# Kernel tuning notes

Hardware: AMD Instinct MI355X
Metric: run time of the kernel (lower is better)

The kernel has to match this reference:

```python
import jax, jax.numpy as jnp
import numpy as np

B, L_SRC, H = 16, 2048, 1024


def setup_inputs() -> dict:
    key = jax.random.key(0)
    ks = jax.random.split(key, 12)
    s = 1.0 / np.sqrt(H)
    return {
        "query": jax.random.normal(ks[0], (B, 1, H), jnp.float32),
        "states": jax.random.normal(ks[1], (B, L_SRC, H), jnp.float32),
        "states_features": jax.random.normal(ks[2], (B, L_SRC, H), jnp.float32),
        "coverage": jax.random.uniform(ks[3], (B, L_SRC, 1), jnp.float32),
        "source_mask": jax.random.randint(ks[4], (B, L_SRC), 0, 2, jnp.int32),
        "is_coverage": 1,
        "Wq": jax.random.normal(ks[5], (H, H), jnp.float32) * s,
        "bq": jax.random.normal(ks[6], (H,), jnp.float32) * s,
        "Wc": jax.random.normal(ks[7], (1, H), jnp.float32) * s,
        "v": jax.random.normal(ks[8], (H, 1), jnp.float32) * s,
        "Wout": jax.random.normal(ks[9], (H, 2 * H), jnp.float32) * s,
        "bout": jax.random.normal(ks[10], (H,), jnp.float32) * s,
    }


def reference(query, states, states_features, coverage, source_mask, is_coverage,
              Wq, bq, Wc, v, Wout, bout):
    # query: (B,1,H); states/states_features: (B,L,H); coverage: (B,L,1)
    query_features = query @ Wq.T + bq                       # (B,1,H), broadcasts over L
    total = query_features + states_features                 # (B,L,H)
    if is_coverage:
        total = total + coverage @ Wc                        # Linear(1,H), no bias
    alignments = jnp.tanh(total) @ v                         # (B,L,1)
    mask = source_mask.astype(bool)[:, :, None]              # (B,L,1)
    alignments = jnp.where(mask, alignments, -jnp.inf)
    align_vectors = jax.nn.softmax(alignments, axis=1)       # softmax over L_src
    c = jnp.einsum('bls,blh->bsh', align_vectors, states)    # (B,1,H)
    concat_c = jnp.concatenate([c, query], axis=2)           # (B,1,2H)
    attn_h = concat_c @ Wout.T + bout                         # (B,1,H)
    new_coverage = coverage + align_vectors
    return attn_h, new_coverage, align_vectors
```

## Files before the change

kernel.cpp:

```cpp
#include <hip/hip_runtime.h>
#include <cfloat>

#define HD 1024
#define LS 2048
#define NB 16
#define NCH 128
#define LPER (LS / NCH)

struct f4 { float x, y, z, w; };

__device__ inline f4 ld4(const float* p) { return *reinterpret_cast<const f4*>(p); }

__device__ inline float ftanh(float x) {
    x = fminf(10.f, fmaxf(-10.f, x));
    float t = __expf(2.f * x);
    return 1.f - 2.f * __builtin_amdgcn_rcpf(t + 1.f);
}

__device__ inline float dotTanh(const f4& s, const f4& q, const f4& wc, const f4& v, float covs) {
    return ftanh(s.x + q.x + covs * wc.x) * v.x
         + ftanh(s.y + q.y + covs * wc.y) * v.y
         + ftanh(s.z + q.z + covs * wc.z) * v.z
         + ftanh(s.w + q.w + covs * wc.w) * v.w;
}

__device__ inline float waveReduce(float v) {
    #pragma unroll
    for (int off = 32; off; off >>= 1) v += __shfl_xor(v, off, 64);
    return v;
}

__global__ void qf_kernel(const float* __restrict__ query, const float* __restrict__ Wq,
                          const float* __restrict__ bq, float* __restrict__ qf) {
    int h = blockIdx.x;
    int tid = threadIdx.x;
    int wv = tid >> 6, lane = tid & 63;
    int k0 = tid * 4;
    f4 w = ld4(Wq + (size_t)h * HD + k0);
    __shared__ float red[4][NB];
    float acc[NB];
    #pragma unroll
    for (int b = 0; b < NB; ++b) {
        f4 q = ld4(query + b * HD + k0);
        acc[b] = w.x * q.x + w.y * q.y + w.z * q.z + w.w * q.w;
    }
    #pragma unroll
    for (int b = 0; b < NB; ++b) {
        float r = waveReduce(acc[b]);
        if (lane == 0) red[wv][b] = r;
    }
    __syncthreads();
    if (tid < NB) {
        float s = red[0][tid] + red[1][tid] + red[2][tid] + red[3][tid];
        qf[tid * HD + h] = s + bq[h];
    }
}

__global__ __launch_bounds__(256) void fusedEC_kernel(
    const float* __restrict__ sf, const float* __restrict__ qf,
    const float* __restrict__ Wc, const float* __restrict__ vv,
    const float* __restrict__ coverage, const int* __restrict__ mask,
    const int* __restrict__ is_cov_p, const float* __restrict__ states,
    float* __restrict__ e_out, float* __restrict__ cpart)
{
    int chunk = blockIdx.x;
    int b = blockIdx.y;
    int tid = threadIdx.x;
    int wv = tid >> 6, lane = tid & 63;
    int l4 = lane * 4;
    int base_row = b * LS + chunk * LPER;
    int row0 = base_row + wv * 4;

    __shared__ float e_loc[LPER];

    int covflag = *is_cov_p;
    int4 mk = *reinterpret_cast<const int4*>(mask + row0);
    bool m0 = mk.x != 0, m1 = mk.y != 0, m2 = mk.z != 0, m3 = mk.w != 0;
    float cov0 = (covflag && m0) ? coverage[row0 + 0] : 0.f;
    float cov1 = (covflag && m1) ? coverage[row0 + 1] : 0.f;
    float cov2 = (covflag && m2) ? coverage[row0 + 2] : 0.f;
    float cov3 = (covflag && m3) ? coverage[row0 + 3] : 0.f;

    const float* qfr = qf + b * HD + l4;
    const float* ps = sf + (size_t)row0 * HD + l4;
    float a0 = 0.f, a1 = 0.f, a2 = 0.f, a3 = 0.f;

    #pragma unroll
    for (int it = 0; it < 4; ++it) {
        int o = it * 256;
        f4 q  = ld4(qfr + o);
        f4 wc = ld4(Wc + o + l4);
        f4 vf = ld4(vv + o + l4);
        f4 s0, s1, s2, s3;
        if (m0) s0 = ld4(ps + o);
        if (m1) s1 = ld4(ps + HD + o);
        if (m2) s2 = ld4(ps + 2 * HD + o);
        if (m3) s3 = ld4(ps + 3 * HD + o);
        if (m0) a0 += dotTanh(s0, q, wc, vf, cov0);
        if (m1) a1 += dotTanh(s1, q, wc, vf, cov1);
        if (m2) a2 += dotTanh(s2, q, wc, vf, cov2);
        if (m3) a3 += dotTanh(s3, q, wc, vf, cov3);
    }

    #pragma unroll
    for (int off = 32; off; off >>= 1) {
        a0 += __shfl_xor(a0, off, 64);
        a1 += __shfl_xor(a1, off, 64);
        a2 += __shfl_xor(a2, off, 64);
        a3 += __shfl_xor(a3, off, 64);
    }
    if (lane == 0) {
        f4 o;
        o.x = m0 ? a0 : -1e30f;
        o.y = m1 ? a1 : -1e30f;
        o.z = m2 ? a2 : -1e30f;
        o.w = m3 ? a3 : -1e30f;
        *reinterpret_cast<f4*>(e_out + row0) = o;
        e_loc[wv * 4 + 0] = o.x;
        e_loc[wv * 4 + 1] = o.y;
        e_loc[wv * 4 + 2] = o.z;
        e_loc[wv * 4 + 3] = o.w;
    }
    __syncthreads();

    __shared__ float wq[LPER];
    __shared__ int ridx[LPER];
    __shared__ int snnz;
    if (tid < 64) {
        float ev = (tid < LPER) ? e_loc[tid] : -1e30f;
        float w = __expf(ev);
        unsigned long long bm = __ballot(w != 0.f);
        if (w != 0.f) {
            int pos = __popcll(bm & ((1ull << tid) - 1));
            wq[pos] = w;
            ridx[pos] = tid;
        }
        if (tid == 0) snnz = __popcll(bm);
    }
    __syncthreads();
    int nnz = snnz;
    int h0 = tid * 4;
    const float* sbase = states + (size_t)base_row * HD + h0;
    float ax = 0.f, ay = 0.f, az = 0.f, aw = 0.f;
    for (int i = 0; i < nnz; i += 4) {
        int j1 = i + 1, j2 = i + 2, j3 = i + 3;
        float w0 = wq[i];
        int   r0 = ridx[i];
        float w1 = (j1 < nnz) ? wq[j1] : 0.f;
        int   r1 = (j1 < nnz) ? ridx[j1] : r0;
        float w2 = (j2 < nnz) ? wq[j2] : 0.f;
        int   r2 = (j2 < nnz) ? ridx[j2] : r0;
        float w3 = (j3 < nnz) ? wq[j3] : 0.f;
        int   r3 = (j3 < nnz) ? ridx[j3] : r0;
        f4 s0 = ld4(sbase + ((size_t)r0 << 10));
        f4 s1 = ld4(sbase + ((size_t)r1 << 10));
        f4 s2 = ld4(sbase + ((size_t)r2 << 10));
        f4 s3 = ld4(sbase + ((size_t)r3 << 10));
        ax = fmaf(w0, s0.x, ax); ay = fmaf(w0, s0.y, ay); az = fmaf(w0, s0.z, az); aw = fmaf(w0, s0.w, aw);
        ax = fmaf(w1, s1.x, ax); ay = fmaf(w1, s1.y, ay); az = fmaf(w1, s1.z, az); aw = fmaf(w1, s1.w, aw);
        ax = fmaf(w2, s2.x, ax); ay = fmaf(w2, s2.y, ay); az = fmaf(w2, s2.z, az); aw = fmaf(w2, s2.w, aw);
        ax = fmaf(w3, s3.x, ax); ay = fmaf(w3, s3.y, ay); az = fmaf(w3, s3.z, az); aw = fmaf(w3, s3.w, aw);
    }
    f4 o; o.x = ax; o.y = ay; o.z = az; o.w = aw;
    *reinterpret_cast<f4*>(cpart + ((size_t)(b * NCH + chunk)) * HD + h0) = o;
}

__global__ __launch_bounds__(1024) void mid_kernel(
    const float* __restrict__ e, const float* __restrict__ coverage,
    const float* __restrict__ cpart, float* __restrict__ scale,
    float* __restrict__ csum, float* __restrict__ out_align, float* __restrict__ out_newcov)
{
    __shared__ float redm[16], reds[16];
    __shared__ float red4[4][256];
    if (blockIdx.x < 16) {
        int b = blockIdx.x;
        int t = threadIdx.x;
        int wv = t >> 6, lane = t & 63;
        float v0 = e[b * LS + t];
        float v1 = e[b * LS + t + 1024];
        float mx = fmaxf(v0, v1);
        #pragma unroll
        for (int off = 32; off; off >>= 1) mx = fmaxf(mx, __shfl_xor(mx, off, 64));
        if (lane == 0) redm[wv] = mx;
        __syncthreads();
        mx = redm[0];
        #pragma unroll
        for (int i = 1; i < 16; ++i) mx = fmaxf(mx, redm[i]);
        float e0 = __expf(v0 - mx), e1 = __expf(v1 - mx);
        float s = e0 + e1;
        #pragma unroll
        for (int off = 32; off; off >>= 1) s += __shfl_xor(s, off, 64);
        if (lane == 0) reds[wv] = s;
        __syncthreads();
        s = 0.f;
        #pragma unroll
        for (int i = 0; i < 16; ++i) s += reds[i];
        float invZ = 1.f / s;
        if (t == 0) scale[b] = __expf(-mx) * invZ;
        int i0 = b * LS + t, i1 = i0 + 1024;
        float p0 = e0 * invZ, p1 = e1 * invZ;
        out_align[i0] = p0;
        out_align[i1] = p1;
        out_newcov[i0] = coverage[i0] + p0;
        out_newcov[i1] = coverage[i1] + p1;
    } else {
        int blk = blockIdx.x - 16;
        int tt = threadIdx.x & 255;
        int g = threadIdx.x >> 8;
        int elem = blk * 256 + tt;
        int b = elem >> 10, h = elem & 1023;
        const float* p = cpart + (((size_t)(b * NCH + g * 32)) << 10) + h;
        float s = 0.f;
        #pragma unroll
        for (int ch = 0; ch < 32; ++ch) s += p[(size_t)ch << 10];
        red4[g][tt] = s;
        __syncthreads();
        if (g == 0) csum[elem] = red4[0][tt] + red4[1][tt] + red4[2][tt] + red4[3][tt];
    }
}

__global__ void out_kernel(const float* __restrict__ csum, const float* __restrict__ query,
                           const float* __restrict__ Wout, const float* __restrict__ bout,
                           const float* __restrict__ scale, float* __restrict__ attn) {
    int h = blockIdx.x;
    int tid = threadIdx.x;
    int wv = tid >> 6, lane = tid & 63;
    int j0 = tid * 8;
    const float* wr = Wout + (size_t)h * (2 * HD);
    f4 w0 = ld4(wr + j0);
    f4 w1 = ld4(wr + j0 + 4);
    const float* src = (j0 < HD) ? (csum + j0) : (query + j0 - HD);
    __shared__ float red[4][NB];
    float acc[NB];
    #pragma unroll
    for (int b = 0; b < NB; ++b) {
        f4 x0 = ld4(src + b * HD);
        f4 x1 = ld4(src + b * HD + 4);
        acc[b] = w0.x * x0.x + w0.y * x0.y + w0.z * x0.z + w0.w * x0.w
               + w1.x * x1.x + w1.y * x1.y + w1.z * x1.z + w1.w * x1.w;
    }
    #pragma unroll
    for (int b = 0; b < NB; ++b) {
        float r = waveReduce(acc[b]);
        if (lane == 0) red[wv][b] = r;
    }
    __syncthreads();
    if (tid < NB) {
        float cpartial = red[0][tid] + red[1][tid];
        float qpartial = red[2][tid] + red[3][tid];
        attn[tid * HD + h] = cpartial * scale[tid] + qpartial + bout[h];
    }
}

extern "C" void kernel_launch(void* const* d_in, const int* in_sizes, int n_in,
                              void* d_out, int out_size, void* d_ws, size_t ws_size,
                              hipStream_t stream) {
    const float* query    = (const float*)d_in[0];
    const float* states   = (const float*)d_in[1];
    const float* sf       = (const float*)d_in[2];
    const float* coverage = (const float*)d_in[3];
    const int*   mask     = (const int*)d_in[4];
    const int*   is_cov   = (const int*)d_in[5];
    const float* Wq       = (const float*)d_in[6];
    const float* bq       = (const float*)d_in[7];
    const float* Wc       = (const float*)d_in[8];
    const float* v        = (const float*)d_in[9];
    const float* Wout     = (const float*)d_in[10];
    const float* bout     = (const float*)d_in[11];

    float* out      = (float*)d_out;
    float* attn     = out;
    float* newcov   = out + 16384;
    float* alignout = out + 49152;

    float* w  = (float*)d_ws;
    float* qf      = w;
    float* e       = w + 16384;
    float* cpart   = w + 49152;
    float* scale   = w + 49152 + 2097152;
    float* csum    = scale + 16;

    qf_kernel<<<dim3(HD), dim3(256), 0, stream>>>(query, Wq, bq, qf);
    fusedEC_kernel<<<dim3(NCH, NB), dim3(256), 0, stream>>>(
        sf, qf, Wc, v, coverage, mask, is_cov, states, e, cpart);
    mid_kernel<<<dim3(80), dim3(1024), 0, stream>>>(e, coverage, cpart, scale, csum, alignout, newcov);
    out_kernel<<<dim3(HD), dim3(256), 0, stream>>>(csum, query, Wout, bout, scale, attn);
}
```

Measured before the change: 56.80 us.

## Stage unmasked feature and state rows into LDS via async global_load_lds

The fused energy/context kernel now reads the mask first, compacts the unmasked row indices, and copies only those rows of states_features into a 64 KB shared buffer using direct global-to-LDS loads. It computes energies from LDS, then reuses the same buffer to stage the needed states rows before the weighted context sum. The aim is to issue the memory traffic asynchronously and in bulk, keeping it off the register path, and to skip masked rows early. The cost is 64 KB of LDS per block, which limits occupancy to about one or two blocks per CU, plus extra barriers that serialize load and compute phases.

```diff
diff --git a/kernel.cpp b/kernel.cpp
--- a/kernel.cpp
+++ b/kernel.cpp
@@ -10,6 +10,13 @@
 struct f4 { float x, y, z, w; };
 
 __device__ inline f4 ld4(const float* p) { return *reinterpret_cast<const f4*>(p); }
+
+__device__ inline void stage16(const float* g, float* l) {
+    __builtin_amdgcn_global_load_lds(
+        (const __attribute__((address_space(1))) void*)g,
+        (__attribute__((address_space(3))) void*)(void*)l,
+        16, 0, 0);
+}
 
 __device__ inline float ftanh(float x) {
     x = fminf(10.f, fmaxf(-10.f, x));
@@ -63,99 +70,93 @@
     const int* __restrict__ is_cov_p, const float* __restrict__ states,
     float* __restrict__ e_out, float* __restrict__ cpart)
 {
+    __shared__ float buf[LPER * HD];
+    __shared__ float e_loc[LPER];
+    __shared__ float ec[LPER];
+    __shared__ float wq[LPER];
+    __shared__ int   ridx[LPER];
+    __shared__ int   snnz;
+
     int chunk = blockIdx.x;
     int b = blockIdx.y;
     int tid = threadIdx.x;
     int wv = tid >> 6, lane = tid & 63;
     int l4 = lane * 4;
     int base_row = b * LS + chunk * LPER;
-    int row0 = base_row + wv * 4;
-
-    __shared__ float e_loc[LPER];
-
-    int covflag = *is_cov_p;
-    int4 mk = *reinterpret_cast<const int4*>(mask + row0);
-    bool m0 = mk.x != 0, m1 = mk.y != 0, m2 = mk.z != 0, m3 = mk.w != 0;
-    float cov0 = (covflag && m0) ? coverage[row0 + 0] : 0.f;
-    float cov1 = (covflag && m1) ? coverage[row0 + 1] : 0.f;
-    float cov2 = (covflag && m2) ? coverage[row0 + 2] : 0.f;
-    float cov3 = (covflag && m3) ? coverage[row0 + 3] : 0.f;
-
-    const float* qfr = qf + b * HD + l4;
-    const float* ps = sf + (size_t)row0 * HD + l4;
-    float a0 = 0.f, a1 = 0.f, a2 = 0.f, a3 = 0.f;
-
-    #pragma unroll
-    for (int it = 0; it < 4; ++it) {
-        int o = it * 256;
-        f4 q  = ld4(qfr + o);
-        f4 wc = ld4(Wc + o + l4);
-        f4 vf = ld4(vv + o + l4);
-        f4 s0, s1, s2, s3;
-        if (m0) s0 = ld4(ps + o);
-        if (m1) s1 = ld4(ps + HD + o);
-        if (m2) s2 = ld4(ps + 2 * HD + o);
-        if (m3) s3 = ld4(ps + 3 * HD + o);
-        if (m0) a0 += dotTanh(s0, q, wc, vf, cov0);
-        if (m1) a1 += dotTanh(s1, q, wc, vf, cov1);
-        if (m2) a2 += dotTanh(s2, q, wc, vf, cov2);
-        if (m3) a3 += dotTanh(s3, q, wc, vf, cov3);
-    }
-
-    #pragma unroll
-    for (int off = 32; off; off >>= 1) {
-        a0 += __shfl_xor(a0, off, 64);
-        a1 += __shfl_xor(a1, off, 64);
-        a2 += __shfl_xor(a2, off, 64);
-        a3 += __shfl_xor(a3, off, 64);
-    }
-    if (lane == 0) {
-        f4 o;
-        o.x = m0 ? a0 : -1e30f;
-        o.y = m1 ? a1 : -1e30f;
-        o.z = m2 ? a2 : -1e30f;
-        o.w = m3 ? a3 : -1e30f;
-        *reinterpret_cast<f4*>(e_out + row0) = o;
-        e_loc[wv * 4 + 0] = o.x;
-        e_loc[wv * 4 + 1] = o.y;
-        e_loc[wv * 4 + 2] = o.z;
-        e_loc[wv * 4 + 3] = o.w;
-    }
-    __syncthreads();
-
-    __shared__ float wq[LPER];
-    __shared__ int ridx[LPER];
-    __shared__ int snnz;
+
     if (tid < 64) {
-        float ev = (tid < LPER) ? e_loc[tid] : -1e30f;
-        float w = __expf(ev);
-        unsigned long long bm = __ballot(w != 0.f);
-        if (w != 0.f) {
+        int mk = (tid < LPER) ? mask[base_row + tid] : 0;
+        unsigned long long bm = __ballot(mk != 0);
+        if (tid < LPER) e_loc[tid] = -1e30f;
+        if (mk != 0) {
             int pos = __popcll(bm & ((1ull << tid) - 1));
-            wq[pos] = w;
             ridx[pos] = tid;
         }
         if (tid == 0) snnz = __popcll(bm);
     }
     __syncthreads();
     int nnz = snnz;
+
+    for (int i = wv; i < nnz; i += 4) {
+        const float* src = sf + (size_t)(base_row + ridx[i]) * HD + l4;
+        float* dst = &buf[i * HD];
+        stage16(src,       dst);
+        stage16(src + 256, dst + 256);
+        stage16(src + 512, dst + 512);
+        stage16(src + 768, dst + 768);
+    }
+
+    const float* qfr = qf + b * HD + l4;
+    f4 q0 = ld4(qfr),      q1 = ld4(qfr + 256),      q2 = ld4(qfr + 512),      q3 = ld4(qfr + 768);
+    f4 c0 = ld4(Wc + l4),  c1 = ld4(Wc + 256 + l4),  c2 = ld4(Wc + 512 + l4),  c3 = ld4(Wc + 768 + l4);
+    f4 v0 = ld4(vv + l4),  v1 = ld4(vv + 256 + l4),  v2 = ld4(vv + 512 + l4),  v3 = ld4(vv + 768 + l4);
+    int covflag = *is_cov_p;
+
+    __syncthreads();
+
+    for (int i = wv; i < nnz; i += 4) {
+        int r = ridx[i];
+        float covs = covflag ? coverage[base_row + r] : 0.f;
+        const float* rp = &buf[i * HD + l4];
+        float a = dotTanh(ld4(rp),       q0, c0, v0, covs)
+                + dotTanh(ld4(rp + 256), q1, c1, v1, covs)
+                + dotTanh(ld4(rp + 512), q2, c2, v2, covs)
+                + dotTanh(ld4(rp + 768), q3, c3, v3, covs);
+        a = waveReduce(a);
+        if (lane == 0) { ec[i] = a; e_loc[r] = a; }
+    }
+    __syncthreads();
+
+    for (int i = wv; i < nnz; i += 4) {
+        const float* src = states + (size_t)(base_row + ridx[i]) * HD + l4;
+        float* dst = &buf[i * HD];
+        stage16(src,       dst);
+        stage16(src + 256, dst + 256);
+        stage16(src + 512, dst + 512);
+        stage16(src + 768, dst + 768);
+    }
+    if (tid < LPER) {
+        e_out[base_row + tid] = e_loc[tid];
+        if (tid < nnz) wq[tid] = __expf(ec[tid]);
+    }
+    __syncthreads();
+
     int h0 = tid * 4;
-    const float* sbase = states + (size_t)base_row * HD + h0;
+    const float* bp = &buf[h0];
     float ax = 0.f, ay = 0.f, az = 0.f, aw = 0.f;
     for (int i = 0; i < nnz; i += 4) {
         int j1 = i + 1, j2 = i + 2, j3 = i + 3;
         float w0 = wq[i];
-        int   r0 = ridx[i];
         float w1 = (j1 < nnz) ? wq[j1] : 0.f;
-        int   r1 = (j1 < nnz) ? ridx[j1] : r0;
         float w2 = (j2 < nnz) ? wq[j2] : 0.f;
-        int   r2 = (j2 < nnz) ? ridx[j2] : r0;
         float w3 = (j3 < nnz) ? wq[j3] : 0.f;
-        int   r3 = (j3 < nnz) ? ridx[j3] : r0;
-        f4 s0 = ld4(sbase + ((size_t)r0 << 10));
-        f4 s1 = ld4(sbase + ((size_t)r1 << 10));
-        f4 s2 = ld4(sbase + ((size_t)r2 << 10));
-        f4 s3 = ld4(sbase + ((size_t)r3 << 10));
+        int r1 = (j1 < nnz) ? j1 : 0;
+        int r2 = (j2 < nnz) ? j2 : 0;
+        int r3 = (j3 < nnz) ? j3 : 0;
+        f4 s0 = ld4(bp + ((size_t)i  << 10));
+        f4 s1 = ld4(bp + ((size_t)r1 << 10));
+        f4 s2 = ld4(bp + ((size_t)r2 << 10));
+        f4 s3 = ld4(bp + ((size_t)r3 << 10));
         ax = fmaf(w0, s0.x, ax); ay = fmaf(w0, s0.y, ay); az = fmaf(w0, s0.z, az); aw = fmaf(w0, s0.w, aw);
         ax = fmaf(w1, s1.x, ax); ay = fmaf(w1, s1.y, ay); az = fmaf(w1, s1.z, az); aw = fmaf(w1, s1.w, aw);
         ax = fmaf(w2, s2.x, ax); ay = fmaf(w2, s2.y, ay); az = fmaf(w2, s2.z, az); aw = fmaf(w2, s2.w, aw);
```

Result: slower. 60.59 us (+6.7%).
